# Optimization experiments

Hardware: AMD Instinct MI355X
Metric: run time of the kernel (lower is better)

## Reference

```python
import jax, jax.numpy as jnp
import numpy as np
from jax import lax

V_SZ, E_DIM, H_SZ = 32000, 256, 1024
BATCH, SEQ = 8, 512


def setup_inputs() -> dict:
    key = jax.random.key(0)
    ks = jax.random.split(key, 12)
    x = jax.random.randint(ks[0], (BATCH, SEQ), 0, V_SZ)
    emb = jax.random.normal(ks[1], (V_SZ, E_DIM), dtype=jnp.float32)
    # layer 0: input E_DIM -> H_SZ
    W_ih0 = jax.random.normal(ks[2], (E_DIM, H_SZ), dtype=jnp.float32) / np.sqrt(E_DIM)
    b_ih0 = jnp.zeros((H_SZ,), jnp.float32)
    W_hh0 = jax.random.normal(ks[3], (H_SZ, H_SZ), dtype=jnp.float32) / np.sqrt(H_SZ)
    b_hh0 = jnp.zeros((H_SZ,), jnp.float32)
    # layer 1: input H_SZ -> H_SZ
    W_ih1 = jax.random.normal(ks[4], (H_SZ, H_SZ), dtype=jnp.float32) / np.sqrt(H_SZ)
    b_ih1 = jnp.zeros((H_SZ,), jnp.float32)
    W_hh1 = jax.random.normal(ks[5], (H_SZ, H_SZ), dtype=jnp.float32) / np.sqrt(H_SZ)
    b_hh1 = jnp.zeros((H_SZ,), jnp.float32)
    # output projection (nn.Linear: y = x @ W.T + b); store as [H_SZ, V_SZ]
    lim = 1.0 / np.sqrt(H_SZ)
    W_out = jax.random.uniform(ks[6], (H_SZ, V_SZ), jnp.float32, -lim, lim)
    b_out = jax.random.uniform(ks[7], (V_SZ,), jnp.float32, -lim, lim)
    return {
        'x': x, 'emb': emb,
        'W_ih0': W_ih0, 'b_ih0': b_ih0, 'W_hh0': W_hh0, 'b_hh0': b_hh0,
        'W_ih1': W_ih1, 'b_ih1': b_ih1, 'W_hh1': W_hh1, 'b_hh1': b_hh1,
        'W_out': W_out, 'b_out': b_out,
    }


def reference(x, emb, W_ih0, b_ih0, W_hh0, b_hh0,
              W_ih1, b_ih1, W_hh1, b_hh1, W_out, b_out):
    B, S = x.shape
    embeds = emb[x]  # [B, S, E]
    h0_init = jnp.zeros((B, H_SZ), embeds.dtype)
    h1_init = jnp.zeros((B, H_SZ), embeds.dtype)

    def step(carry, e_t):
        h0, h1 = carry
        # Elman cell per layer: tanh(x@W_ih + b_ih + h@W_hh + b_hh)
        h0 = jnp.tanh(e_t @ W_ih0 + b_ih0 + h0 @ W_hh0 + b_hh0)
        # dropout is identity in eval/inference reference
        h1 = jnp.tanh(h0 @ W_ih1 + b_ih1 + h1 @ W_hh1 + b_hh1)
        return (h0, h1), h1

    (h0, h1), outs = lax.scan(step, (h0_init, h1_init),
                              jnp.transpose(embeds, (1, 0, 2)))  # outs: [S, B, H]
    outs = jnp.transpose(outs, (1, 0, 2))  # [B, S, H]
    logits = outs @ W_out + b_out  # [B, S, V]
    return logits, h0, h1
```

## Files before the change

### kernel.cpp

```cpp
#include <hip/hip_runtime.h>

#define AS1 __attribute__((address_space(1)))
#define AS3 __attribute__((address_space(3)))

typedef __attribute__((ext_vector_type(4))) float f32x4;
typedef __attribute__((ext_vector_type(8))) short s16x8;

__device__ __forceinline__ void gl_lds16(void* lds, const void* g) {
    __builtin_amdgcn_global_load_lds((const AS1 unsigned int*)g,
                                     (AS3 unsigned int*)lds, 16, 0, 0);
}

__device__ __forceinline__ unsigned short f2bf(float f) {
    unsigned int u = __float_as_uint(f);
    u = (u + 0x7FFFu + ((u >> 16) & 1u)) >> 16;
    return (unsigned short)u;
}

__global__ __launch_bounds__(256) void k_x0(const int* __restrict__ x,
                                            const float* __restrict__ emb,
                                            const float* __restrict__ Wih0,
                                            const float* __restrict__ bih0,
                                            const float* __restrict__ bhh0,
                                            float* __restrict__ X0) {
    __shared__ float elds[16][256];
    const int tid = threadIdx.x, blk = blockIdx.x;
    const int r0 = blk * 16;
    {
        const int rr = tid >> 4, sg = tid & 15;
        const int r = r0 + rr, tt = r >> 3, bb = r & 7;
        const int tok = x[bb * 512 + tt];
        const float4* ep = (const float4*)(emb + (size_t)tok * 256);
        float4* el = (float4*)(&elds[rr][0]);
#pragma unroll
        for (int j = 0; j < 4; ++j) el[sg * 4 + j] = ep[sg * 4 + j];
    }
    __syncthreads();
    float acc[16][4];
#pragma unroll
    for (int a = 0; a < 16; ++a) { acc[a][0]=0.f; acc[a][1]=0.f; acc[a][2]=0.f; acc[a][3]=0.f; }
    const int c0 = tid * 4;
    for (int k = 0; k < 256; ++k) {
        const float4 w = *(const float4*)(Wih0 + (size_t)k * 1024 + c0);
#pragma unroll
        for (int a = 0; a < 16; ++a) {
            const float e = elds[a][k];
            acc[a][0] += e * w.x; acc[a][1] += e * w.y;
            acc[a][2] += e * w.z; acc[a][3] += e * w.w;
        }
    }
    const float4 bi = *(const float4*)(bih0 + c0);
    const float4 bh = *(const float4*)(bhh0 + c0);
#pragma unroll
    for (int a = 0; a < 16; ++a) {
        float4 o;
        o.x = acc[a][0] + bi.x + bh.x; o.y = acc[a][1] + bi.y + bh.y;
        o.z = acc[a][2] + bi.z + bh.z; o.w = acc[a][3] + bi.w + bh.w;
        *(float4*)(X0 + (size_t)(r0 + a) * 1024 + c0) = o;
    }
}

__global__ __launch_bounds__(256) void k_wt(const float* __restrict__ W,
                                            unsigned short* __restrict__ WT) {
    __shared__ unsigned short lt[128 * 136];
    const int tid = threadIdx.x;
    const int kt = blockIdx.x / 250, nt = blockIdx.x % 250;
    const int krow = tid >> 5, ncol = (tid & 31) * 4;
    for (int it = 0; it < 16; ++it) {
        const int kl = it * 8 + krow;
        const float4 v = *(const float4*)(W + (size_t)(kt * 128 + kl) * 32000 + nt * 128 + ncol);
        lt[(ncol + 0) * 136 + kl] = f2bf(v.x);
        lt[(ncol + 1) * 136 + kl] = f2bf(v.y);
        lt[(ncol + 2) * 136 + kl] = f2bf(v.z);
        lt[(ncol + 3) * 136 + kl] = f2bf(v.w);
    }
    __syncthreads();
    const int sg = tid & 15;
    for (int ot = 0; ot < 8; ++ot) {
        const int nl = ot * 16 + (tid >> 4);
        const uint4 u = *(uint4*)&lt[nl * 136 + sg * 8];
        *(uint4*)(WT + (size_t)(nt * 128 + nl) * 1024 + kt * 128 + sg * 8) = u;
    }
}

__global__ __launch_bounds__(256) void k_scan(
    const float* __restrict__ X0, float* __restrict__ H0, float* __restrict__ H1,
    unsigned short* __restrict__ H1b,
    const float* __restrict__ Whh0, const float* __restrict__ Wih1,
    const float* __restrict__ Whh1,
    const float* __restrict__ bih1, const float* __restrict__ bhh1,
    int* __restrict__ cnt0, int* __restrict__ cnt1,
    float* __restrict__ oh0, float* __restrict__ oh1) {
    __shared__ float smem[20736];
    float* hl0  = smem;
    float* hl1  = smem + 8192;
    float* part = smem + 16384;
    const int tid = threadIdx.x, bid = blockIdx.x;
    const int wv = tid >> 6, lid = tid & 63;

    if (bid < 64) {
        const int j = bid, c0 = j * 16;
        const int ks = tid >> 3, cp = tid & 7;
        float2 w[32];
#pragma unroll
        for (int i = 0; i < 32; ++i)
            w[i] = *(const float2*)(Whh0 + (size_t)(i * 32 + ks) * 1024 + c0 + cp * 2);
        const int rb = tid & 7, rc = tid >> 3;

        for (int t = 0; t < 512; ++t) {
            float xv = 0.f;
            if (tid < 128) xv = X0[(size_t)(t * 8 + rb) * 1024 + c0 + rc];
            if (t > 0 && wv == 0) {
                int v = __hip_atomic_load(&cnt0[t - 1], __ATOMIC_RELAXED, __HIP_MEMORY_SCOPE_AGENT);
                while (v < 64) {
                    __builtin_amdgcn_s_sleep(1);
                    v = __hip_atomic_load(&cnt0[t - 1], __ATOMIC_RELAXED, __HIP_MEMORY_SCOPE_AGENT);
                }
            }
            asm volatile("" ::: "memory");
            __syncthreads();
            {
                const float* src = H0 + (size_t)t * 8192;
#pragma unroll
                for (int q = 0; q < 8; ++q) {
                    const int ch = wv * 8 + q;
                    gl_lds16(hl0 + ch * 256, src + ch * 256 + lid * 4);
                }
            }
            __syncthreads();
            float y0[8], y1[8];
#pragma unroll
            for (int b = 0; b < 8; ++b) { y0[b] = 0.f; y1[b] = 0.f; }
#pragma unroll
            for (int i = 0; i < 32; ++i) {
                const int k = i * 32 + ks;
                const float4 ha = *(const float4*)(hl0 + (k << 3));
                const float4 hb = *(const float4*)(hl0 + (k << 3) + 4);
                const float wa = w[i].x, wb = w[i].y;
                y0[0] += ha.x * wa; y0[1] += ha.y * wa; y0[2] += ha.z * wa; y0[3] += ha.w * wa;
                y0[4] += hb.x * wa; y0[5] += hb.y * wa; y0[6] += hb.z * wa; y0[7] += hb.w * wa;
                y1[0] += ha.x * wb; y1[1] += ha.y * wb; y1[2] += ha.z * wb; y1[3] += ha.w * wb;
                y1[4] += hb.x * wb; y1[5] += hb.y * wb; y1[6] += hb.z * wb; y1[7] += hb.w * wb;
            }
#pragma unroll
            for (int b = 0; b < 8; ++b) {
                part[ks * 136 + (cp * 2 + 0) * 8 + b] = y0[b];
                part[ks * 136 + (cp * 2 + 1) * 8 + b] = y1[b];
            }
            __syncthreads();
            if (tid < 128) {
                float s = 0.f;
                for (int kr = 0; kr < 32; ++kr) s += part[kr * 136 + rc * 8 + rb];
                s += xv;
                const float hv = tanhf(s);
                __hip_atomic_store(&H0[(size_t)(t + 1) * 8192 + (c0 + rc) * 8 + rb], hv,
                                   __ATOMIC_RELAXED, __HIP_MEMORY_SCOPE_AGENT);
                if (t == 511) oh0[rb * 1024 + c0 + rc] = hv;
            }
            __syncthreads();
            if (tid == 0)
                __hip_atomic_fetch_add(&cnt0[t], 1, __ATOMIC_RELAXED, __HIP_MEMORY_SCOPE_AGENT);
        }
    } else {
        const int j = bid - 64, c0 = j * 8;
        const int ks = tid >> 2, cp = tid & 3;
        float2 wi[16], wh[16];
#pragma unroll
        for (int i = 0; i < 16; ++i) {
            wi[i] = *(const float2*)(Wih1 + (size_t)(i * 64 + ks) * 1024 + c0 + cp * 2);
            wh[i] = *(const float2*)(Whh1 + (size_t)(i * 64 + ks) * 1024 + c0 + cp * 2);
        }
        const int rb = tid & 7, rc = tid >> 3;
        float biasc = 0.f;
        if (tid < 64) biasc = bih1[c0 + rc] + bhh1[c0 + rc];

        for (int t = 0; t < 512; ++t) {
            if (wv == 0) {
                int v = __hip_atomic_load(&cnt0[t], __ATOMIC_RELAXED, __HIP_MEMORY_SCOPE_AGENT);
                while (v < 64) {
                    __builtin_amdgcn_s_sleep(1);
                    v = __hip_atomic_load(&cnt0[t], __ATOMIC_RELAXED, __HIP_MEMORY_SCOPE_AGENT);
                }
            } else if (t > 0 && wv == 1) {
                int v = __hip_atomic_load(&cnt1[t - 1], __ATOMIC_RELAXED, __HIP_MEMORY_SCOPE_AGENT);
                while (v < 128) {
                    __builtin_amdgcn_s_sleep(1);
                    v = __hip_atomic_load(&cnt1[t - 1], __ATOMIC_RELAXED, __HIP_MEMORY_SCOPE_AGENT);
                }
            }
            asm volatile("" ::: "memory");
            __syncthreads();
            {
                const float* s0 = H0 + (size_t)(t + 1) * 8192;
                const float* s1 = H1 + (size_t)t * 8192;
#pragma unroll
                for (int q = 0; q < 8; ++q) {
                    const int ch = wv * 8 + q;
                    gl_lds16(hl0 + ch * 256, s0 + ch * 256 + lid * 4);
                    gl_lds16(hl1 + ch * 256, s1 + ch * 256 + lid * 4);
                }
            }
            __syncthreads();
            float y0[8], y1[8];
#pragma unroll
            for (int b = 0; b < 8; ++b) { y0[b] = 0.f; y1[b] = 0.f; }
#pragma unroll
            for (int i = 0; i < 16; ++i) {
                const int k = i * 64 + ks;
                const float4 ha = *(const float4*)(hl0 + (k << 3));
                const float4 hb = *(const float4*)(hl0 + (k << 3) + 4);
                const float4 ga = *(const float4*)(hl1 + (k << 3));
                const float4 gb = *(const float4*)(hl1 + (k << 3) + 4);
                {   const float wa = wi[i].x, wb = wi[i].y;
                    y0[0] += ha.x * wa; y0[1] += ha.y * wa; y0[2] += ha.z * wa; y0[3] += ha.w * wa;
                    y0[4] += hb.x * wa; y0[5] += hb.y * wa; y0[6] += hb.z * wa; y0[7] += hb.w * wa;
                    y1[0] += ha.x * wb; y1[1] += ha.y * wb; y1[2] += ha.z * wb; y1[3] += ha.w * wb;
                    y1[4] += hb.x * wb; y1[5] += hb.y * wb; y1[6] += hb.z * wb; y1[7] += hb.w * wb; }
                {   const float wa = wh[i].x, wb = wh[i].y;
                    y0[0] += ga.x * wa; y0[1] += ga.y * wa; y0[2] += ga.z * wa; y0[3] += ga.w * wa;
                    y0[4] += gb.x * wa; y0[5] += gb.y * wa; y0[6] += gb.z * wa; y0[7] += gb.w * wa;
                    y1[0] += ga.x * wb; y1[1] += ga.y * wb; y1[2] += ga.z * wb; y1[3] += ga.w * wb;
                    y1[4] += gb.x * wb; y1[5] += gb.y * wb; y1[6] += gb.z * wb; y1[7] += gb.w * wb; }
            }
#pragma unroll
            for (int b = 0; b < 8; ++b) {
                part[ks * 65 + (cp * 2 + 0) * 8 + b] = y0[b];
                part[ks * 65 + (cp * 2 + 1) * 8 + b] = y1[b];
            }
            __syncthreads();
            if (tid < 64) {
                float s = biasc;
                for (int kr = 0; kr < 64; ++kr) s += part[kr * 65 + rc * 8 + rb];
                const float hv = tanhf(s);
                __hip_atomic_store(&H1[(size_t)(t + 1) * 8192 + (c0 + rc) * 8 + rb], hv,
                                   __ATOMIC_RELAXED, __HIP_MEMORY_SCOPE_AGENT);
                H1b[(size_t)(rb * 512 + t) * 1024 + c0 + rc] = f2bf(hv);
                if (t == 511) oh1[rb * 1024 + c0 + rc] = hv;
            }
            __syncthreads();
            if (tid == 0)
                __hip_atomic_fetch_add(&cnt1[t], 1, __ATOMIC_RELAXED, __HIP_MEMORY_SCOPE_AGENT);
        }
    }
}

__global__ __launch_bounds__(256) void k_logits(const unsigned short* __restrict__ A,
                                                const unsigned short* __restrict__ Bt,
                                                const float* __restrict__ bout,
                                                float* __restrict__ C) {
    __shared__ unsigned short Al[128 * 64];
    __shared__ unsigned short Bl[128 * 64];
    const int tid = threadIdx.x;
    const int nt = blockIdx.x % 250, mt = blockIdx.x / 250;
    const size_t m0 = (size_t)mt * 128, n0 = (size_t)nt * 128;
    const int wv = tid >> 6, lane = tid & 63;
    const int wm = wv & 1, wn = wv >> 1;
    const int row8 = lane >> 3, sg = lane & 7;
    const int lr = lane & 15, qd = lane >> 4;

    f32x4 acc[4][4];
#pragma unroll
    for (int mi = 0; mi < 4; ++mi)
#pragma unroll
        for (int ni = 0; ni < 4; ++ni) acc[mi][ni] = (f32x4)(0.f);

    for (int kb = 0; kb < 16; ++kb) {
#pragma unroll
        for (int q = 0; q < 4; ++q) {
            const int rbase = wv * 32 + q * 8;
            gl_lds16(Al + rbase * 64, A + (m0 + rbase + row8) * 1024 + kb * 64 + sg * 8);
            gl_lds16(Bl + rbase * 64, Bt + (n0 + rbase + row8) * 1024 + kb * 64 + sg * 8);
        }
        __syncthreads();
#pragma unroll
        for (int kk = 0; kk < 2; ++kk) {
            s16x8 af[4], bfr[4];
#pragma unroll
            for (int mi = 0; mi < 4; ++mi)
                af[mi] = *(const s16x8*)&Al[(wm * 64 + mi * 16 + lr) * 64 + kk * 32 + qd * 8];
#pragma unroll
            for (int ni = 0; ni < 4; ++ni)
                bfr[ni] = *(const s16x8*)&Bl[(wn * 64 + ni * 16 + lr) * 64 + kk * 32 + qd * 8];
#pragma unroll
            for (int mi = 0; mi < 4; ++mi)
#pragma unroll
                for (int ni = 0; ni < 4; ++ni)
                    acc[mi][ni] = __builtin_amdgcn_mfma_f32_16x16x32_bf16(af[mi], bfr[ni], acc[mi][ni], 0, 0, 0);
        }
        __syncthreads();
    }
#pragma unroll
    for (int ni = 0; ni < 4; ++ni) {
        const size_t n = n0 + wn * 64 + ni * 16 + lr;
        const float bo = bout[n];
#pragma unroll
        for (int mi = 0; mi < 4; ++mi) {
#pragma unroll
            for (int r = 0; r < 4; ++r) {
                const size_t m = m0 + wm * 64 + mi * 16 + qd * 4 + r;
                C[m * 32000 + n] = acc[mi][ni][r] + bo;
            }
        }
    }
}

extern "C" void kernel_launch(void* const* d_in, const int* in_sizes, int n_in,
                              void* d_out, int out_size, void* d_ws, size_t ws_size,
                              hipStream_t stream) {
    const int* x      = (const int*)d_in[0];
    const float* emb  = (const float*)d_in[1];
    const float* Wih0 = (const float*)d_in[2];
    const float* bih0 = (const float*)d_in[3];
    const float* Whh0 = (const float*)d_in[4];
    const float* bhh0 = (const float*)d_in[5];
    const float* Wih1 = (const float*)d_in[6];
    const float* bih1 = (const float*)d_in[7];
    const float* Whh1 = (const float*)d_in[8];
    const float* bhh1 = (const float*)d_in[9];
    const float* Wout = (const float*)d_in[10];
    const float* bout = (const float*)d_in[11];

    char* ws = (char*)d_ws;
    float* X0           = (float*)(ws + 0);
    float* H0           = (float*)(ws + 16777216);
    float* H1           = (float*)(ws + 33587200);
    unsigned short* H1b = (unsigned short*)(ws + 50397184);
    unsigned short* WT  = (unsigned short*)(ws + 58785792);
    int* cnt0           = (int*)(ws + 124321792);
    int* cnt1           = cnt0 + 512;

    float* out = (float*)d_out;
    float* oh0 = out + 131072000ll;
    float* oh1 = oh0 + 8192;

    hipMemsetAsync(H0, 0, 32768, stream);
    hipMemsetAsync(H1, 0, 32768, stream);
    hipMemsetAsync(cnt0, 0, 4096, stream);

    k_x0<<<256, 256, 0, stream>>>(x, emb, Wih0, bih0, bhh0, X0);
    k_wt<<<2000, 256, 0, stream>>>(Wout, WT);
    k_scan<<<192, 256, 0, stream>>>(X0, H0, H1, H1b, Whh0, Wih1, Whh1,
                                    bih1, bhh1, cnt0, cnt1, oh0, oh1);
    k_logits<<<8000, 256, 0, stream>>>(H1b, WT, bout, out);
}
```

Measured before the change: 2.829 ms.

## Replace per-step atomic counters with per-producer flags polled by every wave

Each producer wave or block in the recurrent scan now writes its own ready flag for each timestep, instead of doing a fetch_add on a shared counter. Every wave polls all 128 flags with a wave-wide 64-bit load and __all, rather than one wave spinning and then releasing the others through __syncthreads. This removes two block barriers and the atomic contention from each of the 512 serial steps. The cost is a larger flag array to memset and more polling traffic, and correctness now depends on relaxed atomics plus an explicit vmcnt wait for ordering.

```diff
diff --git a/kernel.cpp b/kernel.cpp
--- a/kernel.cpp
+++ b/kernel.cpp
@@ -15,6 +15,15 @@
     unsigned int u = __float_as_uint(f);
     u = (u + 0x7FFFu + ((u >> 16) & 1u)) >> 16;
     return (unsigned short)u;
+}
+
+__device__ __forceinline__ void poll128(const int* fp, int lid) {
+    const unsigned long long* p = (const unsigned long long*)fp + lid;
+    for (;;) {
+        unsigned long long v = __hip_atomic_load(p, __ATOMIC_RELAXED, __HIP_MEMORY_SCOPE_AGENT);
+        if (__all(((unsigned)v != 0u) & ((unsigned)(v >> 32) != 0u))) break;
+        __builtin_amdgcn_s_sleep(1);
+    }
 }
 
 __global__ __launch_bounds__(256) void k_x0(const int* __restrict__ x,
@@ -89,7 +98,7 @@
     const float* __restrict__ Whh0, const float* __restrict__ Wih1,
     const float* __restrict__ Whh1,
     const float* __restrict__ bih1, const float* __restrict__ bhh1,
-    int* __restrict__ cnt0, int* __restrict__ cnt1,
+    int* __restrict__ flags0, int* __restrict__ flags1,
     float* __restrict__ oh0, float* __restrict__ oh1) {
     __shared__ float smem[20736];
     float* hl0  = smem;
@@ -110,15 +119,7 @@
         for (int t = 0; t < 512; ++t) {
             float xv = 0.f;
             if (tid < 128) xv = X0[(size_t)(t * 8 + rb) * 1024 + c0 + rc];
-            if (t > 0 && wv == 0) {
-                int v = __hip_atomic_load(&cnt0[t - 1], __ATOMIC_RELAXED, __HIP_MEMORY_SCOPE_AGENT);
-                while (v < 64) {
-                    __builtin_amdgcn_s_sleep(1);
-                    v = __hip_atomic_load(&cnt0[t - 1], __ATOMIC_RELAXED, __HIP_MEMORY_SCOPE_AGENT);
-                }
-            }
-            asm volatile("" ::: "memory");
-            __syncthreads();
+            if (t > 0) poll128(flags0 + (size_t)(t - 1) * 128, lid);
             {
                 const float* src = H0 + (size_t)t * 8192;
 #pragma unroll
@@ -156,10 +157,11 @@
                 __hip_atomic_store(&H0[(size_t)(t + 1) * 8192 + (c0 + rc) * 8 + rb], hv,
                                    __ATOMIC_RELAXED, __HIP_MEMORY_SCOPE_AGENT);
                 if (t == 511) oh0[rb * 1024 + c0 + rc] = hv;
-            }
-            __syncthreads();
-            if (tid == 0)
-                __hip_atomic_fetch_add(&cnt0[t], 1, __ATOMIC_RELAXED, __HIP_MEMORY_SCOPE_AGENT);
+                asm volatile("s_waitcnt vmcnt(0)" ::: "memory");
+                if ((tid & 63) == 0)
+                    __hip_atomic_store(&flags0[(size_t)t * 128 + j * 2 + (tid >> 6)], 1,
+                                       __ATOMIC_RELAXED, __HIP_MEMORY_SCOPE_AGENT);
+            }
         }
     } else {
         const int j = bid - 64, c0 = j * 8;
@@ -175,21 +177,8 @@
         if (tid < 64) biasc = bih1[c0 + rc] + bhh1[c0 + rc];
 
         for (int t = 0; t < 512; ++t) {
-            if (wv == 0) {
-                int v = __hip_atomic_load(&cnt0[t], __ATOMIC_RELAXED, __HIP_MEMORY_SCOPE_AGENT);
-                while (v < 64) {
-                    __builtin_amdgcn_s_sleep(1);
-                    v = __hip_atomic_load(&cnt0[t], __ATOMIC_RELAXED, __HIP_MEMORY_SCOPE_AGENT);
-                }
-            } else if (t > 0 && wv == 1) {
-                int v = __hip_atomic_load(&cnt1[t - 1], __ATOMIC_RELAXED, __HIP_MEMORY_SCOPE_AGENT);
-                while (v < 128) {
-                    __builtin_amdgcn_s_sleep(1);
-                    v = __hip_atomic_load(&cnt1[t - 1], __ATOMIC_RELAXED, __HIP_MEMORY_SCOPE_AGENT);
-                }
-            }
-            asm volatile("" ::: "memory");
-            __syncthreads();
+            if (t > 0) poll128(flags1 + (size_t)(t - 1) * 128, lid);
+            poll128(flags0 + (size_t)t * 128, lid);
             {
                 const float* s0 = H0 + (size_t)(t + 1) * 8192;
                 const float* s1 = H1 + (size_t)t * 8192;
@@ -236,10 +225,11 @@
                                    __ATOMIC_RELAXED, __HIP_MEMORY_SCOPE_AGENT);
                 H1b[(size_t)(rb * 512 + t) * 1024 + c0 + rc] = f2bf(hv);
                 if (t == 511) oh1[rb * 1024 + c0 + rc] = hv;
-            }
-            __syncthreads();
-            if (tid == 0)
-                __hip_atomic_fetch_add(&cnt1[t], 1, __ATOMIC_RELAXED, __HIP_MEMORY_SCOPE_AGENT);
+                asm volatile("s_waitcnt vmcnt(0)" ::: "memory");
+                if (tid == 0)
+                    __hip_atomic_store(&flags1[(size_t)t * 128 + j], 1,
+                                       __ATOMIC_RELAXED, __HIP_MEMORY_SCOPE_AGENT);
+            }
         }
     }
 }
@@ -326,8 +316,8 @@
     float* H1           = (float*)(ws + 33587200);
     unsigned short* H1b = (unsigned short*)(ws + 50397184);
     unsigned short* WT  = (unsigned short*)(ws + 58785792);
-    int* cnt0           = (int*)(ws + 124321792);
-    int* cnt1           = cnt0 + 512;
+    int* flags0         = (int*)(ws + 124321792);
+    int* flags1         = flags0 + 512 * 128;
 
     float* out = (float*)d_out;
     float* oh0 = out + 131072000ll;
@@ -335,11 +325,11 @@
 
     hipMemsetAsync(H0, 0, 32768, stream);
     hipMemsetAsync(H1, 0, 32768, stream);
-    hipMemsetAsync(cnt0, 0, 4096, stream);
+    hipMemsetAsync(flags0, 0, 524288, stream);
 
     k_x0<<<256, 256, 0, stream>>>(x, emb, Wih0, bih0, bhh0, X0);
     k_wt<<<2000, 256, 0, stream>>>(Wout, WT);
     k_scan<<<192, 256, 0, stream>>>(X0, H0, H1, H1b, Whh0, Wih1, Whh1,
-                                    bih1, bhh1, cnt0, cnt1, oh0, oh1);
+                                    bih1, bhh1, flags0, flags1, oh0, oh1);
     k_logits<<<8000, 256, 0, stream>>>(H1b, WT, bout, out);
 }
```

New measurement: 4.141 ms. 1.46x slower.

## Overlap W_out transpose with recurrent scan, coalesce logits stores via LDS

Applied to the files above, without the earlier changes.

The separate bf16 transpose kernel for W_out is removed. Its work now runs in 64 extra blocks of the scan kernel, so it overlaps with the latency-bound recurrence that uses only 192 blocks. The logits GEMM now orders blocks M-fastest so that consecutive blocks share the same W_out tile. Its epilogue stages the accumulators in LDS and writes float4 rows coalesced with the bias added. The extra scan blocks compete for memory bandwidth with the spin-waiting recurrence blocks. The correctness of the scan's spin-wait relies on all 256 blocks being co-resident.

```diff
diff --git a/kernel.cpp b/kernel.cpp
--- a/kernel.cpp
+++ b/kernel.cpp
@@ -60,29 +60,6 @@
     }
 }
 
-__global__ __launch_bounds__(256) void k_wt(const float* __restrict__ W,
-                                            unsigned short* __restrict__ WT) {
-    __shared__ unsigned short lt[128 * 136];
-    const int tid = threadIdx.x;
-    const int kt = blockIdx.x / 250, nt = blockIdx.x % 250;
-    const int krow = tid >> 5, ncol = (tid & 31) * 4;
-    for (int it = 0; it < 16; ++it) {
-        const int kl = it * 8 + krow;
-        const float4 v = *(const float4*)(W + (size_t)(kt * 128 + kl) * 32000 + nt * 128 + ncol);
-        lt[(ncol + 0) * 136 + kl] = f2bf(v.x);
-        lt[(ncol + 1) * 136 + kl] = f2bf(v.y);
-        lt[(ncol + 2) * 136 + kl] = f2bf(v.z);
-        lt[(ncol + 3) * 136 + kl] = f2bf(v.w);
-    }
-    __syncthreads();
-    const int sg = tid & 15;
-    for (int ot = 0; ot < 8; ++ot) {
-        const int nl = ot * 16 + (tid >> 4);
-        const uint4 u = *(uint4*)&lt[nl * 136 + sg * 8];
-        *(uint4*)(WT + (size_t)(nt * 128 + nl) * 1024 + kt * 128 + sg * 8) = u;
-    }
-}
-
 __global__ __launch_bounds__(256) void k_scan(
     const float* __restrict__ X0, float* __restrict__ H0, float* __restrict__ H1,
     unsigned short* __restrict__ H1b,
@@ -90,7 +67,8 @@
     const float* __restrict__ Whh1,
     const float* __restrict__ bih1, const float* __restrict__ bhh1,
     int* __restrict__ cnt0, int* __restrict__ cnt1,
-    float* __restrict__ oh0, float* __restrict__ oh1) {
+    float* __restrict__ oh0, float* __restrict__ oh1,
+    const float* __restrict__ Wout, unsigned short* __restrict__ WT) {
     __shared__ float smem[20736];
     float* hl0  = smem;
     float* hl1  = smem + 8192;
@@ -161,7 +139,7 @@
             if (tid == 0)
                 __hip_atomic_fetch_add(&cnt0[t], 1, __ATOMIC_RELAXED, __HIP_MEMORY_SCOPE_AGENT);
         }
-    } else {
+    } else if (bid < 192) {
         const int j = bid - 64, c0 = j * 8;
         const int ks = tid >> 2, cp = tid & 3;
         float2 wi[16], wh[16];
@@ -241,6 +219,28 @@
             if (tid == 0)
                 __hip_atomic_fetch_add(&cnt1[t], 1, __ATOMIC_RELAXED, __HIP_MEMORY_SCOPE_AGENT);
         }
+    } else {
+        unsigned short* lt = (unsigned short*)smem;
+        for (int tile = bid - 192; tile < 2000; tile += 64) {
+            const int kt = tile / 250, ntw = tile % 250;
+            const int krow = tid >> 5, ncol = (tid & 31) * 4;
+            for (int it = 0; it < 16; ++it) {
+                const int kl = it * 8 + krow;
+                const float4 v = *(const float4*)(Wout + (size_t)(kt * 128 + kl) * 32000 + ntw * 128 + ncol);
+                lt[(ncol + 0) * 136 + kl] = f2bf(v.x);
+                lt[(ncol + 1) * 136 + kl] = f2bf(v.y);
+                lt[(ncol + 2) * 136 + kl] = f2bf(v.z);
+                lt[(ncol + 3) * 136 + kl] = f2bf(v.w);
+            }
+            __syncthreads();
+            const int sg = tid & 15;
+            for (int ot = 0; ot < 8; ++ot) {
+                const int nl = ot * 16 + (tid >> 4);
+                const uint4 u = *(uint4*)&lt[nl * 136 + sg * 8];
+                *(uint4*)(WT + (size_t)(ntw * 128 + nl) * 1024 + kt * 128 + sg * 8) = u;
+            }
+            __syncthreads();
+        }
     }
 }
 
@@ -248,10 +248,12 @@
                                                 const unsigned short* __restrict__ Bt,
                                                 const float* __restrict__ bout,
                                                 float* __restrict__ C) {
-    __shared__ unsigned short Al[128 * 64];
-    __shared__ unsigned short Bl[128 * 64];
+    __shared__ __align__(16) char sbuf[64 * 132 * 4];
+    unsigned short* Al = (unsigned short*)sbuf;
+    unsigned short* Bl = Al + 128 * 64;
+    float* Cst = (float*)sbuf;
     const int tid = threadIdx.x;
-    const int nt = blockIdx.x % 250, mt = blockIdx.x / 250;
+    const int mt = blockIdx.x & 31, nt = blockIdx.x >> 5;
     const size_t m0 = (size_t)mt * 128, n0 = (size_t)nt * 128;
     const int wv = tid >> 6, lane = tid & 63;
     const int wm = wv & 1, wn = wv >> 1;
@@ -289,18 +291,27 @@
         }
         __syncthreads();
     }
-#pragma unroll
-    for (int ni = 0; ni < 4; ++ni) {
-        const size_t n = n0 + wn * 64 + ni * 16 + lr;
-        const float bo = bout[n];
-#pragma unroll
-        for (int mi = 0; mi < 4; ++mi) {
-#pragma unroll
-            for (int r = 0; r < 4; ++r) {
-                const size_t m = m0 + wm * 64 + mi * 16 + qd * 4 + r;
-                C[m * 32000 + n] = acc[mi][ni][r] + bo;
-            }
-        }
+    const int rw0 = tid >> 5;
+    const int c4 = (tid & 31) * 4;
+    const float4 bo4 = *(const float4*)(bout + n0 + c4);
+#pragma unroll
+    for (int h = 0; h < 2; ++h) {
+        if (wm == h) {
+#pragma unroll
+            for (int mi = 0; mi < 4; ++mi)
+#pragma unroll
+                for (int ni = 0; ni < 4; ++ni)
+#pragma unroll
+                    for (int r = 0; r < 4; ++r)
+                        Cst[(mi * 16 + qd * 4 + r) * 132 + wn * 64 + ni * 16 + lr] = acc[mi][ni][r];
+        }
+        __syncthreads();
+        for (int rr = rw0; rr < 64; rr += 8) {
+            float4 v = *(float4*)&Cst[rr * 132 + c4];
+            v.x += bo4.x; v.y += bo4.y; v.z += bo4.z; v.w += bo4.w;
+            *(float4*)(C + (size_t)(m0 + h * 64 + rr) * 32000 + n0 + c4) = v;
+        }
+        __syncthreads();
     }
 }
 
@@ -338,8 +349,7 @@
     hipMemsetAsync(cnt0, 0, 4096, stream);
 
     k_x0<<<256, 256, 0, stream>>>(x, emb, Wih0, bih0, bhh0, X0);
-    k_wt<<<2000, 256, 0, stream>>>(Wout, WT);
-    k_scan<<<192, 256, 0, stream>>>(X0, H0, H1, H1b, Whh0, Wih1, Whh1,
-                                    bih1, bhh1, cnt0, cnt1, oh0, oh1);
+    k_scan<<<256, 256, 0, stream>>>(X0, H0, H1, H1b, Whh0, Wih1, Whh1,
+                                    bih1, bhh1, cnt0, cnt1, oh0, oh1, Wout, WT);
     k_logits<<<8000, 256, 0, stream>>>(H1b, WT, bout, out);
 }
```

After: 2.843 ms. No clear change (+0.5%).

## Overlap W_out transpose with recurrent scan and enlarge logits GEMM tile to 256x128

Applied to the files above, without the earlier changes.

The standalone W_out transpose/bf16-convert kernel is folded into the scan kernel as 64 extra blocks, so that conversion runs concurrently with the latency-bound recurrence on otherwise idle CUs. The logits GEMM now uses 512-thread blocks with a 256x128 output tile, halving the block count and improving B-tile reuse. The risk is that the extra transpose blocks contend for memory bandwidth with the scan's spin-wait synchronization. The larger GEMM block may also lower occupancy.

```diff
diff --git a/kernel.cpp b/kernel.cpp
--- a/kernel.cpp
+++ b/kernel.cpp
@@ -60,29 +60,6 @@
     }
 }
 
-__global__ __launch_bounds__(256) void k_wt(const float* __restrict__ W,
-                                            unsigned short* __restrict__ WT) {
-    __shared__ unsigned short lt[128 * 136];
-    const int tid = threadIdx.x;
-    const int kt = blockIdx.x / 250, nt = blockIdx.x % 250;
-    const int krow = tid >> 5, ncol = (tid & 31) * 4;
-    for (int it = 0; it < 16; ++it) {
-        const int kl = it * 8 + krow;
-        const float4 v = *(const float4*)(W + (size_t)(kt * 128 + kl) * 32000 + nt * 128 + ncol);
-        lt[(ncol + 0) * 136 + kl] = f2bf(v.x);
-        lt[(ncol + 1) * 136 + kl] = f2bf(v.y);
-        lt[(ncol + 2) * 136 + kl] = f2bf(v.z);
-        lt[(ncol + 3) * 136 + kl] = f2bf(v.w);
-    }
-    __syncthreads();
-    const int sg = tid & 15;
-    for (int ot = 0; ot < 8; ++ot) {
-        const int nl = ot * 16 + (tid >> 4);
-        const uint4 u = *(uint4*)&lt[nl * 136 + sg * 8];
-        *(uint4*)(WT + (size_t)(nt * 128 + nl) * 1024 + kt * 128 + sg * 8) = u;
-    }
-}
-
 __global__ __launch_bounds__(256) void k_scan(
     const float* __restrict__ X0, float* __restrict__ H0, float* __restrict__ H1,
     unsigned short* __restrict__ H1b,
@@ -90,7 +67,8 @@
     const float* __restrict__ Whh1,
     const float* __restrict__ bih1, const float* __restrict__ bhh1,
     int* __restrict__ cnt0, int* __restrict__ cnt1,
-    float* __restrict__ oh0, float* __restrict__ oh1) {
+    float* __restrict__ oh0, float* __restrict__ oh1,
+    const float* __restrict__ Wout, unsigned short* __restrict__ WT) {
     __shared__ float smem[20736];
     float* hl0  = smem;
     float* hl1  = smem + 8192;
@@ -161,7 +139,7 @@
             if (tid == 0)
                 __hip_atomic_fetch_add(&cnt0[t], 1, __ATOMIC_RELAXED, __HIP_MEMORY_SCOPE_AGENT);
         }
-    } else {
+    } else if (bid < 192) {
         const int j = bid - 64, c0 = j * 8;
         const int ks = tid >> 2, cp = tid & 3;
         float2 wi[16], wh[16];
@@ -241,20 +219,42 @@
             if (tid == 0)
                 __hip_atomic_fetch_add(&cnt1[t], 1, __ATOMIC_RELAXED, __HIP_MEMORY_SCOPE_AGENT);
         }
-    }
-}
-
-__global__ __launch_bounds__(256) void k_logits(const unsigned short* __restrict__ A,
+    } else {
+        unsigned short* lt = (unsigned short*)smem;
+        for (int tile = bid - 192; tile < 2000; tile += 64) {
+            const int kt = tile / 250, ntw = tile % 250;
+            const int krow = tid >> 5, ncol = (tid & 31) * 4;
+            for (int it = 0; it < 16; ++it) {
+                const int kl = it * 8 + krow;
+                const float4 v = *(const float4*)(Wout + (size_t)(kt * 128 + kl) * 32000 + ntw * 128 + ncol);
+                lt[(ncol + 0) * 136 + kl] = f2bf(v.x);
+                lt[(ncol + 1) * 136 + kl] = f2bf(v.y);
+                lt[(ncol + 2) * 136 + kl] = f2bf(v.z);
+                lt[(ncol + 3) * 136 + kl] = f2bf(v.w);
+            }
+            __syncthreads();
+            const int sg = tid & 15;
+            for (int ot = 0; ot < 8; ++ot) {
+                const int nl = ot * 16 + (tid >> 4);
+                const uint4 u = *(uint4*)&lt[nl * 136 + sg * 8];
+                *(uint4*)(WT + (size_t)(ntw * 128 + nl) * 1024 + kt * 128 + sg * 8) = u;
+            }
+            __syncthreads();
+        }
+    }
+}
+
+__global__ __launch_bounds__(512) void k_logits(const unsigned short* __restrict__ A,
                                                 const unsigned short* __restrict__ Bt,
                                                 const float* __restrict__ bout,
                                                 float* __restrict__ C) {
-    __shared__ unsigned short Al[128 * 64];
+    __shared__ unsigned short Al[256 * 64];
     __shared__ unsigned short Bl[128 * 64];
     const int tid = threadIdx.x;
-    const int nt = blockIdx.x % 250, mt = blockIdx.x / 250;
-    const size_t m0 = (size_t)mt * 128, n0 = (size_t)nt * 128;
+    const int nt = blockIdx.x % 250, mt2 = blockIdx.x / 250;
+    const size_t m0 = (size_t)mt2 * 256, n0 = (size_t)nt * 128;
     const int wv = tid >> 6, lane = tid & 63;
-    const int wm = wv & 1, wn = wv >> 1;
+    const int wm = wv >> 1, wn = wv & 1;
     const int row8 = lane >> 3, sg = lane & 7;
     const int lr = lane & 15, qd = lane >> 4;
 
@@ -269,6 +269,10 @@
         for (int q = 0; q < 4; ++q) {
             const int rbase = wv * 32 + q * 8;
             gl_lds16(Al + rbase * 64, A + (m0 + rbase + row8) * 1024 + kb * 64 + sg * 8);
+        }
+#pragma unroll
+        for (int q = 0; q < 2; ++q) {
+            const int rbase = wv * 16 + q * 8;
             gl_lds16(Bl + rbase * 64, Bt + (n0 + rbase + row8) * 1024 + kb * 64 + sg * 8);
         }
         __syncthreads();
@@ -338,8 +342,7 @@
     hipMemsetAsync(cnt0, 0, 4096, stream);
 
     k_x0<<<256, 256, 0, stream>>>(x, emb, Wih0, bih0, bhh0, X0);
-    k_wt<<<2000, 256, 0, stream>>>(Wout, WT);
-    k_scan<<<192, 256, 0, stream>>>(X0, H0, H1, H1b, Whh0, Wih1, Whh1,
-                                    bih1, bhh1, cnt0, cnt1, oh0, oh1);
-    k_logits<<<8000, 256, 0, stream>>>(H1b, WT, bout, out);
-}
+    k_scan<<<256, 256, 0, stream>>>(X0, H0, H1, H1b, Whh0, Wih1, Whh1,
+                                    bih1, bhh1, cnt0, cnt1, oh0, oh1, Wout, WT);
+    k_logits<<<4000, 512, 0, stream>>>(H1b, WT, bout, out);
+}
```

After: 2.707 ms. -4.3%, faster.
